# Kernel optimization log

Measured on AMD Instinct MI355X. Metric: run time of the kernel, lower is better.

The kernel has to match this reference:

```python
import jax, jax.numpy as jnp
import numpy as np

B, S, V, E, H, L = 32, 64, 96, 256, 512, 3
DIN = 2 * H  # padded input width for stacked LSTM weight tensors


def _cell(x, h, c, Wih, Whh, bih, bhh):
    # PyTorch LSTMCell gate order: i, f, g, o
    g = x @ Wih.T + h @ Whh.T + bih + bhh
    i, f, gg, o = jnp.split(g, 4, axis=-1)
    c2 = jax.nn.sigmoid(f) * c + jax.nn.sigmoid(i) * jnp.tanh(gg)
    h2 = jax.nn.sigmoid(o) * jnp.tanh(c2)
    return h2, c2


def _pad_feat(x, d):
    p = d - x.shape[-1]
    return x if p == 0 else jnp.pad(x, ((0, 0),) * (x.ndim - 1) + ((0, p),))


def _run_lstm(xs, Wih, Whh, bih, bhh, reverse):
    # xs: [S, B, Din]
    if reverse:
        xs = xs[::-1]
    b = xs.shape[1]
    init = (jnp.zeros((b, H), xs.dtype), jnp.zeros((b, H), xs.dtype))

    def step(carry, xt):
        h, c = _cell(xt, carry[0], carry[1], Wih, Whh, bih, bhh)
        return (h, c), h

    (h, c), ys = jax.lax.scan(step, init, xs)
    if reverse:
        ys = ys[::-1]
    return ys, h, c


def setup_inputs():
    key = jax.random.key(0)
    ks = jax.random.split(key, 20)
    f = lambda k, shp, s=0.08: jax.random.normal(k, shp, jnp.float32) * s
    return {
        "src": jax.random.randint(ks[0], (B, S), 0, V - 1),  # avoids padding_idx=95
        "trg": jax.random.randint(ks[1], (B, S), 0, V - 1),
        "embedding": f(ks[2], (V, E), 0.5),
        "enc_Wih": f(ks[3], (L, 2, 4 * H, DIN)),
        "enc_Whh": f(ks[4], (L, 2, 4 * H, H)),
        "enc_bih": f(ks[5], (L, 2, 4 * H)),
        "enc_bhh": f(ks[6], (L, 2, 4 * H)),
        "dec_Wih": f(ks[7], (L, 4 * H, DIN)),
        "dec_Whh": f(ks[8], (L, 4 * H, H)),
        "dec_bih": f(ks[9], (L, 4 * H)),
        "dec_bhh": f(ks[10], (L, 4 * H)),
        "attn_W": f(ks[11], (H, 3 * H)),
        "attn_b": f(ks[12], (H,)),
        "attn_v": jax.random.uniform(ks[13], (H,), jnp.float32),
        "proj_W": f(ks[14], (2 * H, E + 2 * H)),
        "proj_b": f(ks[15], (2 * H,)),
        "fc_W": f(ks[16], (V, H)),
        "fc_b": f(ks[17], (V,)),
    }


def _forward(src, trg, embedding, enc_Wih, enc_Whh, enc_bih, enc_bhh,
             dec_Wih, dec_Whh, dec_bih, dec_bhh, attn_W, attn_b, attn_v,
             proj_W, proj_b, fc_W, fc_b):
    emb = embedding[src]                 # [B,S,E]; dropout=identity (eval)
    xs = emb.transpose(1, 0, 2)          # [S,B,E]
    h_sum, c_sum = [], []
    for l in range(L):
        xin = _pad_feat(xs, DIN)         # zero-pad so stacked weights apply; padded cols hit zeros
        yf, hf, cf = _run_lstm(xin, enc_Wih[l, 0], enc_Whh[l, 0], enc_bih[l, 0], enc_bhh[l, 0], False)
        yb, hb, cb = _run_lstm(xin, enc_Wih[l, 1], enc_Whh[l, 1], enc_bih[l, 1], enc_bhh[l, 1], True)
        xs = jnp.concatenate([yf, yb], -1)  # [S,B,2H]
        h_sum.append(hf + hb)
        c_sum.append(cf + cb)            # hidden.view(L,2,B,H).sum(dim=1)
    enc_out = xs.transpose(1, 0, 2)      # [B,S,2H]
    dec_h, dec_c = jnp.stack(h_sum), jnp.stack(c_sum)  # [L,B,H]

    tokens = trg[:, :-1].T               # teacher_forcing_ratio = 1.0 (deterministic)

    def dec_step(carry, tok):
        h, c = carry
        htop = h[-1]                     # [B,H]
        rep = jnp.concatenate([jnp.broadcast_to(htop[:, None, :], (B, S, H)), enc_out], -1)
        energy = jnp.tanh(rep @ attn_W.T + attn_b)               # [B,S,H]
        attn = jax.nn.softmax(jnp.einsum('d,bsd->bs', attn_v, energy), axis=1)
        context = jnp.einsum('bs,bsd->bd', attn, enc_out)        # [B,2H]
        x = jnp.concatenate([embedding[tok], context], -1) @ proj_W.T + proj_b  # [B,2H]
        hs, cs = [], []
        xin = x
        for l in range(L):
            hl, cl = _cell(_pad_feat(xin, DIN), h[l], c[l], dec_Wih[l], dec_Whh[l], dec_bih[l], dec_bhh[l])
            hs.append(hl)
            cs.append(cl)
            xin = hl
        out = xin @ fc_W.T + fc_b        # [B,V]
        return (jnp.stack(hs), jnp.stack(cs)), out

    _, outs = jax.lax.scan(dec_step, (dec_h, dec_c), tokens)     # [S-1,B,V]
    outputs = jnp.concatenate([jnp.zeros((1, B, V), outs.dtype), outs], 0)
    return outputs.transpose(1, 0, 2)    # [B,S,V]; t=0 row is zeros, matching torch


def reference(src, trg, embedding, enc_Wih, enc_Whh, enc_bih, enc_bhh,
              dec_Wih, dec_Whh, dec_bih, dec_bhh, attn_W, attn_b, attn_v,
              proj_W, proj_b, fc_W, fc_b):
    return _forward(src, trg, embedding, enc_Wih, enc_Whh, enc_bih, enc_bhh,
                    dec_Wih, dec_Whh, dec_bih, dec_bhh, attn_W, attn_b, attn_v,
                    proj_W, proj_b, fc_W, fc_b)
```

## Files before the change

### kernel.cpp

```cpp
#include <hip/hip_runtime.h>

#define B_ 32
#define S_ 64
#define V_ 96
#define E_ 256
#define H_ 512
#define L_ 3
#define DIN_ 1024
#define G4_ 2048
#define BH_ (B_*H_)
#define BDIN_ (B_*DIN_)
#define FSTRIDE 16

typedef unsigned short u16;
typedef u16 u16x8 __attribute__((ext_vector_type(8)));

__device__ __forceinline__ float bfu(u16 u){ return __uint_as_float(((unsigned)u) << 16); }
__device__ __forceinline__ u16 f2b(float f){
  unsigned x = __float_as_uint(f);
  unsigned r = (x + 0x7FFFu + ((x >> 16) & 1u)) >> 16;
  return (u16)r;
}
__device__ __forceinline__ float sigm(float x){ return 1.f/(1.f+__expf(-x)); }
__device__ __forceinline__ float bsum(float a){
  #pragma unroll
  for(int off=1; off<64; off<<=1) a += __shfl_xor(a, off);
  return a;
}
__device__ __forceinline__ void stc(float* p, float v){
  __hip_atomic_store(p, v, __ATOMIC_RELAXED, __HIP_MEMORY_SCOPE_AGENT);
}
__device__ __forceinline__ float ldc(const float* p){
  return __hip_atomic_load((float*)p, __ATOMIC_RELAXED, __HIP_MEMORY_SCOPE_AGENT);
}
__device__ __forceinline__ void stci(int* p, int v){
  __hip_atomic_store(p, v, __ATOMIC_RELAXED, __HIP_MEMORY_SCOPE_AGENT);
}
__device__ __forceinline__ int ldci(const int* p){
  return __hip_atomic_load((int*)p, __ATOMIC_RELAXED, __HIP_MEMORY_SCOPE_AGENT);
}
template<int BF> __device__ __forceinline__ float LD(const void* p, size_t i){
  if constexpr(BF) return bfu(((const u16*)p)[i]);
  else             return ((const float*)p)[i];
}
template<int BF> __device__ __forceinline__ float4 LD4(const void* p, size_t i){
  if constexpr(BF){
    const u16* q = (const u16*)p + i;
    ushort4 w = *(const ushort4*)q;
    return make_float4(bfu(w.x), bfu(w.y), bfu(w.z), bfu(w.w));
  } else {
    return *(const float4*)((const float*)p + i);
  }
}

__device__ __forceinline__ void gbar(int* flags, int g){
  __syncthreads();
  if(threadIdx.x < 64){
    if(threadIdx.x == 0) stci(&flags[blockIdx.x*FSTRIDE], g);
    const int i0 = threadIdx.x*4;
    for(;;){
      int f0 = ldci(&flags[(i0+0)*FSTRIDE]);
      int f1 = ldci(&flags[(i0+1)*FSTRIDE]);
      int f2 = ldci(&flags[(i0+2)*FSTRIDE]);
      int f3 = ldci(&flags[(i0+3)*FSTRIDE]);
      bool ok = (f0>=g) && (f1>=g) && (f2>=g) && (f3>=g);
      if(__all(ok)) break;
      __builtin_amdgcn_s_sleep(1);
    }
  }
  __syncthreads();
}

__global__ void k_detect(const void* av, int* flag, int* flags){
  __shared__ int cnt;
  if(threadIdx.x == 0) cnt = 0;
  __syncthreads();
  u16 w = ((const u16*)av)[2*threadIdx.x];
  if(w & 0x8000) atomicAdd(&cnt, 1);
  __syncthreads();
  for(int i=threadIdx.x; i<256*FSTRIDE+16; i+=256) flags[i] = 0;
  if(threadIdx.x == 0) *flag = (cnt <= 8) ? 1 : 0;
}

template<int BF> __device__ void embed_body(const int* __restrict__ src,
                                            const void* __restrict__ emb,
                                            float* __restrict__ X0){
  int idx = blockIdx.x*256 + threadIdx.x;
  int d  = idx & (DIN_-1);
  int sb = idx >> 10;
  int b  = sb & (B_-1);
  int s  = sb >> 5;
  float v = 0.f;
  if(d < E_){
    int tok = src[b*S_ + s];
    v = LD<BF>(emb, (size_t)tok*E_ + d);
  }
  X0[idx] = v;
}
__global__ void k_embed(const int* src, const void* emb, float* X0, const int* fl){
  if(*fl) embed_body<1>(src, emb, X0); else embed_body<0>(src, emb, X0);
}

template<int BF> __device__ void gemm_body(
  const float* __restrict__ A, int lda,
  const void* __restrict__ W, int ldw, size_t woff,
  const void* __restrict__ b1, size_t o1,
  const void* __restrict__ b2, size_t o2,
  float* __restrict__ C, int ldc, int K)
{
  __shared__ float As[16][128];
  __shared__ float Bs[16][64];
  const int tid = threadIdx.x;
  const int m0 = blockIdx.y * 128;
  const int n0 = blockIdx.x * 64;
  const int tx = tid & 15, ty = tid >> 4;
  const int amm = tid & 127, akk = (tid >> 7) * 8;
  const int bnn = tid >> 2,  bkk = (tid & 3) * 4;
  float acc[8][4] = {{0.f}};
  for(int k0 = 0; k0 < K; k0 += 16){
    const float4* ap = (const float4*)(A + (size_t)(m0+amm)*lda + (k0 + akk));
    float4 a0 = ap[0];
    float4 a1 = ap[1];
    float4 wv = LD4<BF>(W, woff + (size_t)(n0+bnn)*ldw + (k0 + bkk));
    As[akk+0][amm]=a0.x; As[akk+1][amm]=a0.y; As[akk+2][amm]=a0.z; As[akk+3][amm]=a0.w;
    As[akk+4][amm]=a1.x; As[akk+5][amm]=a1.y; As[akk+6][amm]=a1.z; As[akk+7][amm]=a1.w;
    Bs[bkk+0][bnn]=wv.x; Bs[bkk+1][bnn]=wv.y;
    Bs[bkk+2][bnn]=wv.z; Bs[bkk+3][bnn]=wv.w;
    __syncthreads();
    #pragma unroll
    for(int kk=0;kk<16;kk++){
      const float4 av0 = *(const float4*)&As[kk][ty*8];
      const float4 av1 = *(const float4*)&As[kk][ty*8+4];
      const float4 bv  = *(const float4*)&Bs[kk][tx*4];
      float am[8] = {av0.x,av0.y,av0.z,av0.w,av1.x,av1.y,av1.z,av1.w};
      float bn[4] = {bv.x,bv.y,bv.z,bv.w};
      #pragma unroll
      for(int i=0;i<8;i++){
        #pragma unroll
        for(int j=0;j<4;j++) acc[i][j] = fmaf(am[i], bn[j], acc[i][j]);
      }
    }
    __syncthreads();
  }
  float bias[4];
  #pragma unroll
  for(int j=0;j<4;j++){
    float bb = 0.f;
    if(b1) bb += LD<BF>(b1, o1 + n0 + tx*4 + j);
    if(b2) bb += LD<BF>(b2, o2 + n0 + tx*4 + j);
    bias[j] = bb;
  }
  #pragma unroll
  for(int i=0;i<8;i++){
    float* cp = C + (size_t)(m0 + ty*8 + i)*ldc + (n0 + tx*4);
    #pragma unroll
    for(int j=0;j<4;j++) cp[j] = acc[i][j] + bias[j];
  }
}
__global__ __launch_bounds__(256) void k_gemm(
  const float* A, int lda, const void* W, int ldw, size_t woff,
  const void* b1, size_t o1, const void* b2, size_t o2,
  float* C, int ldc, int K, const int* fl)
{
  if(*fl) gemm_body<1>(A,lda,W,ldw,woff,b1,o1,b2,o2,C,ldc,K);
  else    gemm_body<0>(A,lda,W,ldw,woff,b1,o1,b2,o2,C,ldc,K);
}

__global__ void k_outzero(void* __restrict__ out, const int* fl){
  int i = blockIdx.x*256 + threadIdx.x;
  if(i < B_*V_){
    int b = i / V_, v = i % V_;
    size_t idx = (size_t)b*(S_*V_) + v;
    if(*fl) ((u16*)out)[idx] = 0;
    else    ((float*)out)[idx] = 0.f;
  }
}

struct EncArgs2 {
  const float* G;
  const void* Whh; size_t oWh;
  float* henc;
  float* cT;
  float* Xout;
  float* dh0;
  float* dcT;
  int l;
  const int* fl;
  int* flags; int gbase;
};

template<int BF>
__device__ void enc2_body(const EncArgs2& a){
  __shared__ float SM[16384];
  const int tid  = threadIdx.x;
  const int w    = (blockIdx.x<<2) + (tid>>6);
  const int lane = tid & 63;
  const int d    = w >> 9;
  const int j    = w & 511;
  int g = a.gbase;

  float wh[4][8];
  #pragma unroll
  for(int gg=0; gg<4; gg++){
    size_t rowh = a.oWh + ((size_t)d*G4_ + (size_t)gg*H_ + j)*H_;
    #pragma unroll
    for(int p=0;p<2;p++){
      float4 v = LD4<BF>(a.Whh, rowh + (lane<<2) + p*256);
      wh[gg][p*4+0]=v.x; wh[gg][p*4+1]=v.y; wh[gg][p*4+2]=v.z; wh[gg][p*4+3]=v.w;
    }
  }
  const int bE = lane & 31;
  const size_t ci = ((size_t)d*H_ + j)*32 + bE;
  float cv = 0.f;

  for(int p=0;p<64;p++){
    const int t = d ? (63-p) : p;
    if(p == 0){
      for(int i=tid<<2; i<BH_; i+=1024) *(float4*)&SM[i] = make_float4(0.f,0.f,0.f,0.f);
    } else {
      const float* hsrc = a.henc + (size_t)((p&63)*2 + d)*BH_;
      for(int i=tid<<2; i<BH_; i+=1024) *(float4*)&SM[i] = *(const float4*)&hsrc[i];
    }
    __syncthreads();

    const float* Gp = a.G + (size_t)(t*B_+bE)*4096 + (size_t)d*G4_ + j;
    float pg0=Gp[0], pg1=Gp[512], pg2=Gp[1024], pg3=Gp[1536];

    float gv0=0.f, gv1=0.f, gv2=0.f, gv3=0.f;
    for(int b=0;b<32;b++){
      float gs[4] = {0.f,0.f,0.f,0.f};
      const float* hp = &SM[(b<<9) + (lane<<2)];
      #pragma unroll
      for(int pp=0;pp<2;pp++){
        float4 hv = *(const float4*)(hp + pp*256);
        float ha[4] = {hv.x,hv.y,hv.z,hv.w};
        #pragma unroll
        for(int gg=0;gg<4;gg++){
          #pragma unroll
          for(int i=0;i<4;i++) gs[gg] = fmaf(ha[i], wh[gg][pp*4+i], gs[gg]);
        }
      }
      #pragma unroll
      for(int gg=0;gg<4;gg++) gs[gg] = bsum(gs[gg]);
      if(lane == b){ gv0=gs[0]; gv1=gs[1]; gv2=gs[2]; gv3=gs[3]; }
    }
    if(lane < 32){
      float gi = gv0+pg0, gf = gv1+pg1, gG = gv2+pg2, go = gv3+pg3;
      float c2 = sigm(gf)*cv + sigm(gi)*tanhf(gG);
      float h2 = sigm(go)*tanhf(c2);
      cv = c2;
      stc(&a.henc[(size_t)(((p+1)&63)*2 + d)*BH_ + (size_t)bE*H_ + j], h2);
      a.Xout[(size_t)(t*B_+bE)*DIN_ + (d<<9) + j] = h2;
    }
    gbar(a.flags, ++g);
  }
  if(lane < 32) stc(&a.cT[ci], cv);
  gbar(a.flags, ++g);
  for(int i = blockIdx.x*256 + tid; i < BH_; i += 65536){
    float hf = a.henc[(size_t)(0*2+0)*BH_ + i];
    float hb = a.henc[(size_t)(0*2+1)*BH_ + i];
    a.dh0[(size_t)a.l*BH_ + i] = hf + hb;
    a.dcT[(size_t)a.l*BH_ + i] = ldc(&a.cT[i]) + ldc(&a.cT[BH_ + i]);
  }
}
__global__ __launch_bounds__(256,2) void k_enc2(EncArgs2 a){
  if(*a.fl) enc2_body<1>(a); else enc2_body<0>(a);
}

struct DecArgs2 {
  const int* trg;
  const void* emb; const void* aW; const void* av; const void* pW; const void* pb;
  const void* dWih; const void* dWhh; const void* dbih; const void* dbhh;
  const void* fW; const void* fb;
  const float* Epre; const float* X3;
  const float* dh0;
  float* dhb;
  float* zb;
  u16*   ctxb;
  float* xpb;
  const float* dcT;
  void* out;
  const int* fl;
  int* flags; int gbase;
};

template<int BF, int CP>
__device__ __forceinline__ void dec2_cell(const DecArgs2& a, float* SM,
    const int t, const int l, const int jp, const int bh, const int bh_blk,
    const int lane, const int tid, int& g, float& cv){
  constexpr int Kx = CP*256;
  constexpr int HB = (CP==4) ? 2 : 1;
  constexpr int NB = 16/HB;
  const float* xsrc = (l==0) ? (a.xpb + (size_t)t*BDIN_ + (size_t)bh_blk*16*DIN_)
                             : (a.dhb + (size_t)((t+1)*3 + (l-1))*BH_ + (size_t)bh_blk*16*H_);
  const float* hsrc = (t==0) ? (a.dh0 + (size_t)l*BH_ + (size_t)bh_blk*16*H_)
                             : (a.dhb + (size_t)(t*3 + l)*BH_ + (size_t)bh_blk*16*H_);
  float wx[4][CP*4];
  float wh[4][8];
  #pragma unroll
  for(int gg=0; gg<4; gg++){
    size_t rowx = ((size_t)l*G4_ + (size_t)gg*H_ + jp)*DIN_;
    #pragma unroll
    for(int p=0;p<CP;p++){
      float4 v = LD4<BF>(a.dWih, rowx + (lane<<2) + p*256);
      wx[gg][p*4+0]=v.x; wx[gg][p*4+1]=v.y; wx[gg][p*4+2]=v.z; wx[gg][p*4+3]=v.w;
    }
    size_t rowh = ((size_t)l*G4_ + (size_t)gg*H_ + jp)*H_;
    #pragma unroll
    for(int p=0;p<2;p++){
      float4 v = LD4<BF>(a.dWhh, rowh + (lane<<2) + p*256);
      wh[gg][p*4+0]=v.x; wh[gg][p*4+1]=v.y; wh[gg][p*4+2]=v.z; wh[gg][p*4+3]=v.w;
    }
  }
  float pg[4];
  {
    size_t bb = (size_t)l*G4_ + jp;
    #pragma unroll
    for(int gg=0;gg<4;gg++)
      pg[gg] = LD<BF>(a.dbih, bb + (size_t)gg*H_) + LD<BF>(a.dbhh, bb + (size_t)gg*H_);
  }
  float gv0=0.f,gv1=0.f,gv2=0.f,gv3=0.f;
  #pragma unroll
  for(int hf=0; hf<HB; hf++){
    const float* xg = xsrc + (size_t)hf*NB*Kx;
    const float* hg = hsrc + (size_t)hf*NB*H_;
    for(int i=tid<<2; i<NB*Kx; i+=1024) *(float4*)&SM[i] = *(const float4*)&xg[i];
    for(int i=tid<<2; i<NB*H_; i+=1024) *(float4*)&SM[NB*Kx + i] = *(const float4*)&hg[i];
    __syncthreads();
    for(int ib2=0; ib2<NB; ib2++){
      const int ib = hf*NB + ib2;
      float gs[4] = {0.f,0.f,0.f,0.f};
      const float* xr = &SM[ib2*Kx + (lane<<2)];
      #pragma unroll
      for(int p=0;p<CP;p++){
        float4 xv = *(const float4*)(xr + p*256);
        float xa[4] = {xv.x,xv.y,xv.z,xv.w};
        #pragma unroll
        for(int gg=0;gg<4;gg++){
          #pragma unroll
          for(int i=0;i<4;i++) gs[gg] = fmaf(xa[i], wx[gg][p*4+i], gs[gg]);
        }
      }
      const float* hr = &SM[NB*Kx + ib2*H_ + (lane<<2)];
      #pragma unroll
      for(int p=0;p<2;p++){
        float4 hv = *(const float4*)(hr + p*256);
        float ha[4] = {hv.x,hv.y,hv.z,hv.w};
        #pragma unroll
        for(int gg=0;gg<4;gg++){
          #pragma unroll
          for(int i=0;i<4;i++) gs[gg] = fmaf(ha[i], wh[gg][p*4+i], gs[gg]);
        }
      }
      #pragma unroll
      for(int gg=0;gg<4;gg++) gs[gg] = bsum(gs[gg]);
      if(lane == ib){ gv0=gs[0]; gv1=gs[1]; gv2=gs[2]; gv3=gs[3]; }
    }
    __syncthreads();
  }
  if(lane < 16){
    const int b = bh*16 + lane;
    float gi = gv0+pg[0], gf = gv1+pg[1], gG = gv2+pg[2], go = gv3+pg[3];
    float c2 = sigm(gf)*cv + sigm(gi)*tanhf(gG);
    float h2 = sigm(go)*tanhf(c2);
    cv = c2;
    stc(&a.dhb[(size_t)((t+1)*3 + l)*BH_ + (size_t)b*H_ + jp], h2);
  }
  gbar(a.flags, ++g);
}

template<int BF>
__device__ void dec2_body(const DecArgs2& a){
  __shared__ float SM[16384];
  const int tid  = threadIdx.x;
  const int w    = (blockIdx.x<<2) + (tid>>6);
  const int lane = tid & 63;
  const int jp   = w & 511;
  const int bh   = w >> 9;
  const int bh_blk = blockIdx.x >> 7;
  int g = a.gbase;

  float cvs[3];
  #pragma unroll
  for(int l=0;l<3;l++)
    cvs[l] = a.dcT[((size_t)l*H_ + jp)*32 + (size_t)bh*16 + (lane&15)];

  for(int t=0; t<64; ++t){
    {
      const float* hs = (t==0) ? (a.dh0 + (size_t)2*BH_ + (size_t)bh_blk*16*H_)
                               : (a.dhb + (size_t)(t*3 + 2)*BH_ + (size_t)bh_blk*16*H_);
      for(int i=tid<<2; i<16*H_; i+=1024) *(float4*)&SM[i] = *(const float4*)&hs[i];
      __syncthreads();
      if(t < 63){
        float wz[8];
        size_t rz = (size_t)jp*1536;
        #pragma unroll
        for(int p=0;p<2;p++){
          float4 v = LD4<BF>(a.aW, rz + (lane<<2) + p*256);
          wz[p*4+0]=v.x; wz[p*4+1]=v.y; wz[p*4+2]=v.z; wz[p*4+3]=v.w;
        }
        for(int ib=0; ib<16; ib++){
          const float* hp = &SM[(ib<<9) + (lane<<2)];
          float acc = 0.f;
          #pragma unroll
          for(int p=0;p<2;p++){
            float4 hv = *(const float4*)(hp + p*256);
            acc = fmaf(hv.x, wz[p*4+0], acc); acc = fmaf(hv.y, wz[p*4+1], acc);
            acc = fmaf(hv.z, wz[p*4+2], acc); acc = fmaf(hv.w, wz[p*4+3], acc);
          }
          acc = bsum(acc);
          if(lane==0) stc(&a.zb[(size_t)t*BH_ + (size_t)(bh*16+ib)*H_ + jp], acc);
        }
      }
      if(t > 0){
        #pragma unroll
        for(int r=0;r<3;r++){
          const int q  = jp + (r<<9);
          const int v_ = q % 96;
          const int ib = q / 96;
          float wf[8];
          size_t rf = (size_t)v_*H_;
          #pragma unroll
          for(int p=0;p<2;p++){
            float4 v = LD4<BF>(a.fW, rf + (lane<<2) + p*256);
            wf[p*4+0]=v.x; wf[p*4+1]=v.y; wf[p*4+2]=v.z; wf[p*4+3]=v.w;
          }
          const float* hp = &SM[(ib<<9) + (lane<<2)];
          float acc = 0.f;
          #pragma unroll
          for(int p=0;p<2;p++){
            float4 hv = *(const float4*)(hp + p*256);
            acc = fmaf(hv.x, wf[p*4+0], acc); acc = fmaf(hv.y, wf[p*4+1], acc);
            acc = fmaf(hv.z, wf[p*4+2], acc); acc = fmaf(hv.w, wf[p*4+3], acc);
          }
          acc = bsum(acc);
          if(lane==0){
            float rr = acc + LD<BF>(a.fb, v_);
            size_t oi = (size_t)(bh*16+ib)*(S_*V_) + (size_t)t*V_ + v_;
            if constexpr(BF) ((u16*)a.out)[oi] = f2b(rr);
            else             ((float*)a.out)[oi] = rr;
          }
        }
      }
    }
    if(t == 63) break;
    gbar(a.flags, ++g);

    if(blockIdx.x < 32){
      const int b = blockIdx.x;
      float* Zs = SM; float* Ss = SM + 512;
      for(int i=tid; i<512; i+=256) Zs[i] = a.zb[(size_t)t*BH_ + (size_t)b*H_ + i];
      __syncthreads();
      float wa[8];
      #pragma unroll
      for(int p=0;p<2;p++){
        float4 v = LD4<BF>(a.av, (lane<<2) + p*256);
        wa[p*4+0]=v.x; wa[p*4+1]=v.y; wa[p*4+2]=v.z; wa[p*4+3]=v.w;
      }
      const int ww = tid>>6;
      for(int s=ww; s<64; s+=4){
        const float* ep = a.Epre + ((size_t)(s*B_ + b))*H_;
        float acc = 0.f;
        #pragma unroll
        for(int p=0;p<2;p++){
          const float4 e4 = *(const float4*)(ep + (lane<<2) + p*256);
          const float4 z4 = *(const float4*)(Zs + (lane<<2) + p*256);
          acc = fmaf(wa[p*4+0], tanhf(e4.x+z4.x), acc);
          acc = fmaf(wa[p*4+1], tanhf(e4.y+z4.y), acc);
          acc = fmaf(wa[p*4+2], tanhf(e4.z+z4.z), acc);
          acc = fmaf(wa[p*4+3], tanhf(e4.w+z4.w), acc);
        }
        acc = bsum(acc);
        if(lane==0) Ss[s] = acc;
      }
      __syncthreads();
      if(tid < 64){
        float vv = Ss[tid];
        float m = vv;
        #pragma unroll
        for(int off=1; off<64; off<<=1) m = fmaxf(m, __shfl_xor(m, off));
        float e = __expf(vv - m);
        float su = e;
        #pragma unroll
        for(int off=1; off<64; off<<=1) su += __shfl_xor(su, off);
        Ss[tid] = e / su;
      }
      __syncthreads();
      for(int d4 = tid<<2; d4 < DIN_; d4 += 1024){
        float a0=0.f,a1=0.f,a2=0.f,a3=0.f;
        const float* xb = a.X3 + (size_t)b*DIN_ + d4;
        for(int s=0;s<64;s++){
          const float pp = Ss[s];
          const float4 xv = *(const float4*)(xb + (size_t)s*BDIN_);
          a0 = fmaf(pp, xv.x, a0); a1 = fmaf(pp, xv.y, a1);
          a2 = fmaf(pp, xv.z, a2); a3 = fmaf(pp, xv.w, a3);
        }
        u16* cp = a.ctxb + (size_t)t*BDIN_ + (size_t)b*DIN_ + d4;
        unsigned lo = (unsigned)f2b(a0) | ((unsigned)f2b(a1)<<16);
        unsigned hi = (unsigned)f2b(a2) | ((unsigned)f2b(a3)<<16);
        stci((int*)cp, (int)lo);
        stci(((int*)cp)+1, (int)hi);
      }
    }
    gbar(a.flags, ++g);

    {
      const u16* cs = a.ctxb + (size_t)t*BDIN_ + (size_t)bh_blk*16*DIN_;
      for(int i=tid*8; i<16*DIN_; i+=2048){
        u16x8 v = *(const u16x8*)(cs + i);
        #pragma unroll
        for(int k=0;k<8;k++) SM[i+k] = bfu(v[k]);
      }
      __syncthreads();
      float wpe[2][4], wpc[2][16];
      #pragma unroll
      for(int jj=0;jj<2;jj++){
        size_t row = (size_t)(jp + (jj<<9))*1280;
        float4 v = LD4<BF>(a.pW, row + (lane<<2));
        wpe[jj][0]=v.x; wpe[jj][1]=v.y; wpe[jj][2]=v.z; wpe[jj][3]=v.w;
        #pragma unroll
        for(int p=0;p<4;p++){
          float4 c4 = LD4<BF>(a.pW, row + 256 + (lane<<2) + p*256);
          wpc[jj][p*4+0]=c4.x; wpc[jj][p*4+1]=c4.y; wpc[jj][p*4+2]=c4.z; wpc[jj][p*4+3]=c4.w;
        }
      }
      const float pb0 = LD<BF>(a.pb, jp);
      const float pb1 = LD<BF>(a.pb, jp+512);
      for(int ib=0; ib<16; ib++){
        const int b = bh*16 + ib;
        const int tok = a.trg[b*S_ + t];
        float4 ev = LD4<BF>(a.emb, (size_t)tok*E_ + (lane<<2));
        float ea[4] = {ev.x, ev.y, ev.z, ev.w};
        float s0=0.f, s1=0.f;
        #pragma unroll
        for(int i=0;i<4;i++){ s0 = fmaf(ea[i], wpe[0][i], s0); s1 = fmaf(ea[i], wpe[1][i], s1); }
        const float* cp = &SM[(ib<<10) + (lane<<2)];
        #pragma unroll
        for(int p=0;p<4;p++){
          float4 c4 = *(const float4*)(cp + p*256);
          float ca[4] = {c4.x,c4.y,c4.z,c4.w};
          #pragma unroll
          for(int i=0;i<4;i++){ s0 = fmaf(ca[i], wpc[0][p*4+i], s0); s1 = fmaf(ca[i], wpc[1][p*4+i], s1); }
        }
        s0 = bsum(s0); s1 = bsum(s1);
        if(lane==0){
          stc(&a.xpb[(size_t)t*BDIN_ + (size_t)b*DIN_ + jp],       s0 + pb0);
          stc(&a.xpb[(size_t)t*BDIN_ + (size_t)b*DIN_ + jp + 512], s1 + pb1);
        }
      }
    }
    gbar(a.flags, ++g);

    dec2_cell<BF,4>(a, SM, t, 0, jp, bh, bh_blk, lane, tid, g, cvs[0]);
    dec2_cell<BF,2>(a, SM, t, 1, jp, bh, bh_blk, lane, tid, g, cvs[1]);
    dec2_cell<BF,2>(a, SM, t, 2, jp, bh, bh_blk, lane, tid, g, cvs[2]);
  }
}
__global__ __launch_bounds__(256,2) void k_dec2(DecArgs2 a){
  if(*a.fl) dec2_body<1>(a); else dec2_body<0>(a);
}

struct EncArgsO {
  const float* G;
  const float* Xin;
  const void* Wih; size_t oWi;
  const void* Whh; size_t oWh;
  const void* bih; size_t obi;
  const void* bhh; size_t obh;
  float* hst; float* cT; float* Xout; float* dh; float* dcT;
  int l; const int* fl; int* flags; int gbase;
};

template<int BF, int CP>
__device__ void encO_body(const EncArgsO& a){
  __shared__ float SM[16384];
  const int tid  = threadIdx.x;
  const int w    = (blockIdx.x<<2) + (tid>>6);
  const int lane = tid & 63;
  const int d    = w >> 9;
  const int j    = w & 511;
  int g = a.gbase;

  float wh[4][8];
  #pragma unroll
  for(int gg=0; gg<4; gg++){
    size_t rowh = a.oWh + ((size_t)d*G4_ + (size_t)gg*H_ + j)*H_;
    #pragma unroll
    for(int p=0;p<2;p++){
      float4 v = LD4<BF>(a.Whh, rowh + (lane<<2) + p*256);
      wh[gg][p*4+0]=v.x; wh[gg][p*4+1]=v.y; wh[gg][p*4+2]=v.z; wh[gg][p*4+3]=v.w;
    }
  }
  float wxf[4][CP?CP*4:1];
  float pbias[4];
  if constexpr(CP>0){
    #pragma unroll
    for(int gg=0; gg<4; gg++){
      size_t rowx = a.oWi + ((size_t)d*G4_ + (size_t)gg*H_ + j)*DIN_;
      #pragma unroll
      for(int p=0;p<CP;p++){
        float4 v = LD4<BF>(a.Wih, rowx + (lane<<2) + p*256);
        wxf[gg][p*4+0]=v.x; wxf[gg][p*4+1]=v.y; wxf[gg][p*4+2]=v.z; wxf[gg][p*4+3]=v.w;
      }
    }
    size_t bb = (size_t)d*G4_ + j;
    #pragma unroll
    for(int gg=0;gg<4;gg++)
      pbias[gg] = LD<BF>(a.bih, a.obi + bb + (size_t)gg*H_)
                + LD<BF>(a.bhh, a.obh + bb + (size_t)gg*H_);
  }
  const int bE = lane & 31;
  const size_t ci = ((size_t)d*H_ + j)*32 + bE;
  float cv = 0.f;
  int cur = 0;
  for(int p=0;p<64;p++){
    const int t = d ? (63-p) : p;
    if(p == 0){
      for(int i=tid<<2; i<BH_; i+=1024) *(float4*)&SM[i] = make_float4(0.f,0.f,0.f,0.f);
    } else {
      const float* hsrc = a.hst + (size_t)((cur<<1)+d)*BH_;
      #pragma unroll 4
      for(int i=tid; i<BH_; i+=256) SM[i] = ldc(hsrc + i);
    }
    __syncthreads();
    float pg[4];
    if constexpr(CP==0){
      const float* Gp = a.G + (size_t)(t*B_+bE)*4096 + (size_t)d*G4_ + j;
      pg[0]=Gp[0]; pg[1]=Gp[512]; pg[2]=Gp[1024]; pg[3]=Gp[1536];
    } else {
      pg[0]=pbias[0]; pg[1]=pbias[1]; pg[2]=pbias[2]; pg[3]=pbias[3];
    }
    const float* xrow = nullptr;
    if constexpr(CP>0) xrow = a.Xin + (size_t)t*B_*DIN_;
    float gv0=0.f, gv1=0.f, gv2=0.f, gv3=0.f;
    for(int b=0;b<32;b++){
      float gs[4] = {0.f,0.f,0.f,0.f};
      const float* hp = &SM[(b<<9) + (lane<<2)];
      #pragma unroll
      for(int pp=0;pp<2;pp++){
        float4 hv = *(const float4*)(hp + pp*256);
        float ha[4] = {hv.x,hv.y,hv.z,hv.w};
        #pragma unroll
        for(int gg=0;gg<4;gg++){
          #pragma unroll
          for(int i=0;i<4;i++) gs[gg] = fmaf(ha[i], wh[gg][pp*4+i], gs[gg]);
        }
      }
      if constexpr(CP>0){
        const float* xr = xrow + (size_t)b*DIN_ + (lane<<2);
        #pragma unroll
        for(int pp=0;pp<CP;pp++){
          float4 xv = *(const float4*)(xr + pp*256);
          float xa[4] = {xv.x,xv.y,xv.z,xv.w};
          #pragma unroll
          for(int gg=0;gg<4;gg++){
            #pragma unroll
            for(int i=0;i<4;i++) gs[gg] = fmaf(xa[i], wxf[gg][pp*4+i], gs[gg]);
          }
        }
      }
      #pragma unroll
      for(int gg=0;gg<4;gg++) gs[gg] = bsum(gs[gg]);
      if(lane == b){ gv0=gs[0]; gv1=gs[1]; gv2=gs[2]; gv3=gs[3]; }
    }
    if(lane < 32){
      float gi = gv0+pg[0], gf = gv1+pg[1], gG = gv2+pg[2], go = gv3+pg[3];
      float c2 = sigm(gf)*cv + sigm(gi)*tanhf(gG);
      float h2 = sigm(go)*tanhf(c2);
      cv = c2;
      stc(&a.hst[(size_t)(((cur^1)<<1)+d)*BH_ + (size_t)bE*H_ + j], h2);
      a.Xout[(size_t)(t*B_+bE)*DIN_ + (d<<9) + j] = h2;
    }
    gbar(a.flags, ++g);
    cur ^= 1;
  }
  if(lane < 32) stc(&a.cT[ci], cv);
  gbar(a.flags, ++g);
  for(int i = blockIdx.x*256 + tid; i < BH_; i += 65536){
    a.dh[(size_t)a.l*BH_ + i]  = ldc(&a.hst[(size_t)(cur<<1)*BH_ + i])
                               + ldc(&a.hst[(size_t)((cur<<1)+1)*BH_ + i]);
    a.dcT[(size_t)a.l*BH_ + i] = ldc(&a.cT[i]) + ldc(&a.cT[BH_ + i]);
  }
}
__global__ __launch_bounds__(256,2) void k_enc_persF0(EncArgsO a){
  if(*a.fl) encO_body<1,1>(a); else encO_body<0,1>(a);
}
__global__ __launch_bounds__(256,2) void k_enc_persF12(EncArgsO a){
  if(*a.fl) encO_body<1,4>(a); else encO_body<0,4>(a);
}

struct DecArgsO {
  const int* trg;
  const void* emb; const void* aW; const void* av; const void* pW; const void* pb;
  const void* dWih; const void* dWhh; const void* dbih; const void* dbhh;
  const void* fW; const void* fb;
  const float* Epre; const float* X3;
  float* dh; float* dcT; float* z; float* ctx; float* xp;
  void* out; const int* fl; int* flags; int gbase;
};

template<int BF, int CP>
__device__ __forceinline__ void decO_cell(const DecArgsO& a, float* SM,
    const int l, const int cur, const int jp, const int bh, const int bh_blk,
    const int lane, const int tid, int& g, float& cv){
  constexpr int Kx = CP*256;
  constexpr int HB = (CP==4) ? 2 : 1;
  constexpr int NB = 16/HB;
  const float* xsrc = (l==0) ? (a.xp + (size_t)bh_blk*16*DIN_)
                             : (a.dh + ((size_t)(cur^1)*3 + (l-1))*BH_ + (size_t)bh_blk*16*H_);
  const float* hsrc = a.dh + ((size_t)cur*3 + l)*BH_ + (size_t)bh_blk*16*H_;
  float wx[4][CP*4];
// ... 166 lines not shown
        for(int p=0;p<2;p++){
          const float4 e4 = *(const float4*)(ep + (lane<<2) + p*256);
          const float4 z4 = *(const float4*)(Zs + (lane<<2) + p*256);
          acc = fmaf(wa[p*4+0], tanhf(e4.x+z4.x), acc);
          acc = fmaf(wa[p*4+1], tanhf(e4.y+z4.y), acc);
          acc = fmaf(wa[p*4+2], tanhf(e4.z+z4.z), acc);
          acc = fmaf(wa[p*4+3], tanhf(e4.w+z4.w), acc);
        }
        acc = bsum(acc);
        if(lane==0) Ss[s] = acc;
      }
      __syncthreads();
      if(tid < 64){
        float vv = Ss[tid];
        float m = vv;
        #pragma unroll
        for(int off=1; off<64; off<<=1) m = fmaxf(m, __shfl_xor(m, off));
        float e = __expf(vv - m);
        float su = e;
        #pragma unroll
        for(int off=1; off<64; off<<=1) su += __shfl_xor(su, off);
        Ss[tid] = e / su;
      }
      __syncthreads();
      for(int d4 = tid<<2; d4 < DIN_; d4 += 1024){
        float a0=0.f,a1=0.f,a2=0.f,a3=0.f;
        const float* xb = a.X3 + (size_t)b*DIN_ + d4;
        for(int s=0;s<64;s++){
          const float pp = Ss[s];
          const float4 xv = *(const float4*)(xb + (size_t)s*BDIN_);
          a0 = fmaf(pp, xv.x, a0); a1 = fmaf(pp, xv.y, a1);
          a2 = fmaf(pp, xv.z, a2); a3 = fmaf(pp, xv.w, a3);
        }
        float* cp = &a.ctx[(size_t)b*DIN_ + d4];
        stc(cp+0, a0); stc(cp+1, a1); stc(cp+2, a2); stc(cp+3, a3);
      }
    }
    gbar(a.flags, ++g);
    {
      const float* cs = a.ctx + (size_t)bh_blk*16*DIN_;
      #pragma unroll 4
      for(int i=tid; i<16*DIN_; i+=256) SM[i] = ldc(cs + i);
      __syncthreads();
      float wpe[2][4], wpc[2][16];
      #pragma unroll
      for(int jj=0;jj<2;jj++){
        size_t row = (size_t)(jp + (jj<<9))*1280;
        float4 v = LD4<BF>(a.pW, row + (lane<<2));
        wpe[jj][0]=v.x; wpe[jj][1]=v.y; wpe[jj][2]=v.z; wpe[jj][3]=v.w;
        #pragma unroll
        for(int p=0;p<4;p++){
          float4 c4 = LD4<BF>(a.pW, row + 256 + (lane<<2) + p*256);
          wpc[jj][p*4+0]=c4.x; wpc[jj][p*4+1]=c4.y; wpc[jj][p*4+2]=c4.z; wpc[jj][p*4+3]=c4.w;
        }
      }
      const float pb0 = LD<BF>(a.pb, jp);
      const float pb1 = LD<BF>(a.pb, jp+512);
      for(int ib=0; ib<16; ib++){
        const int b = bh*16 + ib;
        const int tok = a.trg[b*S_ + t];
        float4 ev = LD4<BF>(a.emb, (size_t)tok*E_ + (lane<<2));
        float ea[4] = {ev.x, ev.y, ev.z, ev.w};
        float s0=0.f, s1=0.f;
        #pragma unroll
        for(int i=0;i<4;i++){ s0 = fmaf(ea[i], wpe[0][i], s0); s1 = fmaf(ea[i], wpe[1][i], s1); }
        const float* cp = &SM[(ib<<10) + (lane<<2)];
        #pragma unroll
        for(int p=0;p<4;p++){
          float4 c4 = *(const float4*)(cp + p*256);
          float ca[4] = {c4.x,c4.y,c4.z,c4.w};
          #pragma unroll
          for(int i=0;i<4;i++){ s0 = fmaf(ca[i], wpc[0][p*4+i], s0); s1 = fmaf(ca[i], wpc[1][p*4+i], s1); }
        }
        s0 = bsum(s0); s1 = bsum(s1);
        if(lane==0){
          stc(&a.xp[(size_t)b*DIN_ + jp],       s0 + pb0);
          stc(&a.xp[(size_t)b*DIN_ + jp + 512], s1 + pb1);
        }
      }
    }
    gbar(a.flags, ++g);
    decO_cell<BF,4>(a, SM, 0, cur, jp, bh, bh_blk, lane, tid, g, cvs[0]);
    decO_cell<BF,2>(a, SM, 1, cur, jp, bh, bh_blk, lane, tid, g, cvs[1]);
    decO_cell<BF,2>(a, SM, 2, cur, jp, bh, bh_blk, lane, tid, g, cvs[2]);
    cur ^= 1;
  }
}
__global__ __launch_bounds__(256,2) void k_dec_persO(DecArgsO a){
  if(*a.fl) decO_body<1>(a); else decO_body<0>(a);
}

extern "C" void kernel_launch(void* const* d_in, const int* in_sizes, int n_in,
                              void* d_out, int out_size, void* d_ws, size_t ws_size,
                              hipStream_t stream){
  const int* src  = (const int*)d_in[0];
  const int* trg  = (const int*)d_in[1];
  const void* emb = d_in[2];
  const void* eWih= d_in[3];
  const void* eWhh= d_in[4];
  const void* ebih= d_in[5];
  const void* ebhh= d_in[6];
  const void* dWih= d_in[7];
  const void* dWhh= d_in[8];
  const void* dbih= d_in[9];
  const void* dbhh= d_in[10];
  const void* aW  = d_in[11];
  const void* ab  = d_in[12];
  const void* av  = d_in[13];
  const void* pW  = d_in[14];
  const void* pb  = d_in[15];
  const void* fW  = d_in[16];
  const void* fb  = d_in[17];

  char* base = (char*)d_ws;
  size_t off = 0;
  auto take = [&](size_t bytes)->char*{
    char* p = base + off; off = (off + bytes + 255) & ~(size_t)255; return p;
  };

  const size_t szX  = (size_t)2048*1024*4;
  const size_t szG  = (size_t)2048*4096*4;
  const size_t szE  = (size_t)2048*512*4;
  int planA = ws_size >= (size_t)53*1024*1024;

  if(planA){
    float* X    = (float*)take(szX);
    float* Xh   = (float*)take(szX);
    float* G    = (float*)take(szG);
    float* dhb  = G;
    float* zb   = dhb + (size_t)64*3*BH_;
    float* xpb  = zb  + (size_t)63*BH_;
    u16*   ctxb = (u16*)(xpb + (size_t)63*BDIN_);
    float* Epre = (float*)take(szE);
    float* cTe  = (float*)take((size_t)2*BH_*4);
    float* dh0  = (float*)take((size_t)3*BH_*4);
    float* dcT  = (float*)take((size_t)3*BH_*4);
    int* fl     = (int*)take(256);
    int* flags  = (int*)take((256*FSTRIDE + 16)*4);

    k_detect<<<1, 256, 0, stream>>>(av, fl, flags);
    k_embed<<<8192, 256, 0, stream>>>(src, emb, X, fl);

    for(int l=0;l<L_;l++){
      int K = (l==0) ? E_ : DIN_;
      k_gemm<<<dim3(64,16), 256, 0, stream>>>(X, DIN_,
          eWih, DIN_, (size_t)l*2*G4_*DIN_,
          ebih, (size_t)l*2*G4_, ebhh, (size_t)l*2*G4_,
          G, 4096, K, fl);
      EncArgs2 ea;
      ea.G = G; ea.Whh = eWhh; ea.oWh = (size_t)l*2*G4_*H_;
      ea.henc = Xh; ea.cT = cTe; ea.Xout = X;
      ea.dh0 = dh0; ea.dcT = dcT; ea.l = l;
      ea.fl = fl; ea.flags = flags; ea.gbase = l*65;
      k_enc2<<<256, 256, 0, stream>>>(ea);
    }
    k_gemm<<<dim3(8,16), 256, 0, stream>>>(X, DIN_,
        aW, 3*H_, (size_t)H_, ab, 0, nullptr, 0, Epre, H_, DIN_, fl);
    k_outzero<<<12, 256, 0, stream>>>(d_out, fl);

    DecArgs2 da;
    da.trg = trg; da.emb = emb; da.aW = aW; da.av = av; da.pW = pW; da.pb = pb;
    da.dWih = dWih; da.dWhh = dWhh; da.dbih = dbih; da.dbhh = dbhh;
    da.fW = fW; da.fb = fb;
    da.Epre = Epre; da.X3 = X;
    da.dh0 = dh0; da.dhb = dhb; da.zb = zb; da.ctxb = ctxb; da.xpb = xpb;
    da.dcT = dcT; da.out = d_out; da.fl = fl; da.flags = flags; da.gbase = 3*65;
    k_dec2<<<256, 256, 0, stream>>>(da);
  } else {
    float* XA   = (float*)take(szX);
    float* XB   = (float*)take(szX);
    float* Epre = (float*)take(szE);
    float* hst  = (float*)take((size_t)4*BH_*4);
    float* cTe  = (float*)take((size_t)2*BH_*4);
    float* dh   = (float*)take((size_t)6*BH_*4);
    float* dcT  = (float*)take((size_t)3*BH_*4);
    float* zbuf = (float*)take((size_t)BH_*4);
    float* ctx  = (float*)take((size_t)2*BH_*4);
    float* xp   = (float*)take((size_t)2*BH_*4);
    int* fl     = (int*)take(256);
    int* flags  = (int*)take((256*FSTRIDE + 16)*4);

    k_detect<<<1, 256, 0, stream>>>(av, fl, flags);
    k_embed<<<8192, 256, 0, stream>>>(src, emb, XA, fl);

    float* Xin = XA; float* Xout = XB;
    for(int l=0;l<L_;l++){
      int K = (l==0) ? E_ : DIN_;
      EncArgsO ea;
      ea.G = nullptr; ea.Xin = Xin;
      ea.Wih = eWih; ea.oWi = (size_t)l*2*G4_*DIN_;
      ea.Whh = eWhh; ea.oWh = (size_t)l*2*G4_*H_;
      ea.bih = ebih; ea.obi = (size_t)l*2*G4_;
      ea.bhh = ebhh; ea.obh = (size_t)l*2*G4_;
      ea.hst = hst; ea.cT = cTe; ea.Xout = Xout;
      ea.dh = dh; ea.dcT = dcT; ea.l = l;
      ea.fl = fl; ea.flags = flags; ea.gbase = l*65;
      if(l == 0) k_enc_persF0<<<256, 256, 0, stream>>>(ea);
      else       k_enc_persF12<<<256, 256, 0, stream>>>(ea);
      float* tmp = Xin; Xin = Xout; Xout = tmp;
      (void)K;
    }
    k_gemm<<<dim3(8,16), 256, 0, stream>>>(Xin, DIN_,
        aW, 3*H_, (size_t)H_, ab, 0, nullptr, 0, Epre, H_, DIN_, fl);
    k_outzero<<<12, 256, 0, stream>>>(d_out, fl);

    DecArgsO da;
    da.trg = trg; da.emb = emb; da.aW = aW; da.av = av; da.pW = pW; da.pb = pb;
    da.dWih = dWih; da.dWhh = dWhh; da.dbih = dbih; da.dbhh = dbhh;
    da.fW = fW; da.fb = fb;
    da.Epre = Epre; da.X3 = Xin;
    da.dh = dh; da.dcT = dcT; da.z = zbuf; da.ctx = ctx; da.xp = xp;
    da.out = d_out; da.fl = fl; da.flags = flags; da.gbase = 3*65;
    k_dec_persO<<<256, 256, 0, stream>>>(da);
  }
}
```

Before: 11.46 ms.

## Double block size in persistent encoder/decoder, splitting batch rows across wave halves

```diff
diff --git a/kernel.cpp b/kernel.cpp
--- a/kernel.cpp
+++ b/kernel.cpp
@@ -13,7 +13,6 @@
 #define FSTRIDE 16
 
 typedef unsigned short u16;
-typedef u16 u16x8 __attribute__((ext_vector_type(8)));
 
 __device__ __forceinline__ float bfu(u16 u){ return __uint_as_float(((unsigned)u) << 16); }
 __device__ __forceinline__ u16 f2b(float f){
@@ -193,10 +192,12 @@
 __device__ void enc2_body(const EncArgs2& a){
   __shared__ float SM[16384];
   const int tid  = threadIdx.x;
-  const int w    = (blockIdx.x<<2) + (tid>>6);
   const int lane = tid & 63;
-  const int d    = w >> 9;
-  const int j    = w & 511;
+  const int wid  = tid >> 6;
+  const int w4   = (blockIdx.x<<2) + (wid & 3);
+  const int j    = w4 & 511;
+  const int d    = w4 >> 9;
+  const int half = wid >> 2;
   int g = a.gbase;
 
   float wh[4][8];
@@ -209,25 +210,26 @@
       wh[gg][p*4+0]=v.x; wh[gg][p*4+1]=v.y; wh[gg][p*4+2]=v.z; wh[gg][p*4+3]=v.w;
     }
   }
-  const int bE = lane & 31;
-  const size_t ci = ((size_t)d*H_ + j)*32 + bE;
+  const bool own = (lane < 32) && ((lane>>4) == half);
+  const size_t ci = ((size_t)d*H_ + j)*32 + (lane & 31);
   float cv = 0.f;
 
   for(int p=0;p<64;p++){
     const int t = d ? (63-p) : p;
     if(p == 0){
-      for(int i=tid<<2; i<BH_; i+=1024) *(float4*)&SM[i] = make_float4(0.f,0.f,0.f,0.f);
+      for(int i=tid<<2; i<BH_; i+=2048) *(float4*)&SM[i] = make_float4(0.f,0.f,0.f,0.f);
     } else {
       const float* hsrc = a.henc + (size_t)((p&63)*2 + d)*BH_;
-      for(int i=tid<<2; i<BH_; i+=1024) *(float4*)&SM[i] = *(const float4*)&hsrc[i];
+      for(int i=tid<<2; i<BH_; i+=2048) *(float4*)&SM[i] = *(const float4*)&hsrc[i];
     }
     __syncthreads();
 
+    const int bE = lane & 31;
     const float* Gp = a.G + (size_t)(t*B_+bE)*4096 + (size_t)d*G4_ + j;
     float pg0=Gp[0], pg1=Gp[512], pg2=Gp[1024], pg3=Gp[1536];
 
     float gv0=0.f, gv1=0.f, gv2=0.f, gv3=0.f;
-    for(int b=0;b<32;b++){
+    for(int b=half*16; b<half*16+16; b++){
       float gs[4] = {0.f,0.f,0.f,0.f};
       const float* hp = &SM[(b<<9) + (lane<<2)];
       #pragma unroll
@@ -244,26 +246,26 @@
       for(int gg=0;gg<4;gg++) gs[gg] = bsum(gs[gg]);
       if(lane == b){ gv0=gs[0]; gv1=gs[1]; gv2=gs[2]; gv3=gs[3]; }
     }
-    if(lane < 32){
+    if(own){
       float gi = gv0+pg0, gf = gv1+pg1, gG = gv2+pg2, go = gv3+pg3;
       float c2 = sigm(gf)*cv + sigm(gi)*tanhf(gG);
       float h2 = sigm(go)*tanhf(c2);
       cv = c2;
-      stc(&a.henc[(size_t)(((p+1)&63)*2 + d)*BH_ + (size_t)bE*H_ + j], h2);
-      a.Xout[(size_t)(t*B_+bE)*DIN_ + (d<<9) + j] = h2;
+      stc(&a.henc[(size_t)(((p+1)&63)*2 + d)*BH_ + (size_t)lane*H_ + j], h2);
+      a.Xout[(size_t)(t*B_+lane)*DIN_ + (d<<9) + j] = h2;
     }
     gbar(a.flags, ++g);
   }
-  if(lane < 32) stc(&a.cT[ci], cv);
+  if(own) stc(&a.cT[ci], cv);
   gbar(a.flags, ++g);
-  for(int i = blockIdx.x*256 + tid; i < BH_; i += 65536){
-    float hf = a.henc[(size_t)(0*2+0)*BH_ + i];
-    float hb = a.henc[(size_t)(0*2+1)*BH_ + i];
-    a.dh0[(size_t)a.l*BH_ + i] = hf + hb;
+  for(int i = blockIdx.x*512 + tid; i < BH_; i += 131072){
+    float hf2 = a.henc[(size_t)(0*2+0)*BH_ + i];
+    float hb2 = a.henc[(size_t)(0*2+1)*BH_ + i];
+    a.dh0[(size_t)a.l*BH_ + i] = hf2 + hb2;
     a.dcT[(size_t)a.l*BH_ + i] = ldc(&a.cT[i]) + ldc(&a.cT[BH_ + i]);
   }
 }
-__global__ __launch_bounds__(256,2) void k_enc2(EncArgs2 a){
+__global__ __launch_bounds__(512,1) void k_enc2(EncArgs2 a){
   if(*a.fl) enc2_body<1>(a); else enc2_body<0>(a);
 }
 
@@ -287,10 +289,11 @@
 template<int BF, int CP>
 __device__ __forceinline__ void dec2_cell(const DecArgs2& a, float* SM,
     const int t, const int l, const int jp, const int bh, const int bh_blk,
-    const int lane, const int tid, int& g, float& cv){
-  constexpr int Kx = CP*256;
-  constexpr int HB = (CP==4) ? 2 : 1;
-  constexpr int NB = 16/HB;
+    const int lane, const int tid, const int half, int& g, float& cv){
+  constexpr int Kx  = CP*256;
+  constexpr int HB  = (CP==4) ? 2 : 1;
+  constexpr int NBs = 16/HB;
+  constexpr int NW  = NBs/2;
   const float* xsrc = (l==0) ? (a.xpb + (size_t)t*BDIN_ + (size_t)bh_blk*16*DIN_)
                              : (a.dhb + (size_t)((t+1)*3 + (l-1))*BH_ + (size_t)bh_blk*16*H_);
   const float* hsrc = (t==0) ? (a.dh0 + (size_t)l*BH_ + (size_t)bh_blk*16*H_)
@@ -322,13 +325,13 @@
   float gv0=0.f,gv1=0.f,gv2=0.f,gv3=0.f;
   #pragma unroll
   for(int hf=0; hf<HB; hf++){
-    const float* xg = xsrc + (size_t)hf*NB*Kx;
-    const float* hg = hsrc + (size_t)hf*NB*H_;
-    for(int i=tid<<2; i<NB*Kx; i+=1024) *(float4*)&SM[i] = *(const float4*)&xg[i];
-    for(int i=tid<<2; i<NB*H_; i+=1024) *(float4*)&SM[NB*Kx + i] = *(const float4*)&hg[i];
+    const float* xg = xsrc + (size_t)hf*NBs*Kx;
+    const float* hg = hsrc + (size_t)hf*NBs*H_;
+    for(int i=tid<<2; i<NBs*Kx; i+=2048) *(float4*)&SM[i] = *(const float4*)&xg[i];
+    for(int i=tid<<2; i<NBs*H_; i+=2048) *(float4*)&SM[NBs*Kx + i] = *(const float4*)&hg[i];
     __syncthreads();
-    for(int ib2=0; ib2<NB; ib2++){
-      const int ib = hf*NB + ib2;
+    for(int ib2=half*NW; ib2<half*NW+NW; ib2++){
+      const int ib = hf*NBs + ib2;
       float gs[4] = {0.f,0.f,0.f,0.f};
       const float* xr = &SM[ib2*Kx + (lane<<2)];
       #pragma unroll
@@ -341,7 +344,7 @@
           for(int i=0;i<4;i++) gs[gg] = fmaf(xa[i], wx[gg][p*4+i], gs[gg]);
         }
       }
-      const float* hr = &SM[NB*Kx + ib2*H_ + (lane<<2)];
+      const float* hr = &SM[NBs*Kx + ib2*H_ + (lane<<2)];
       #pragma unroll
       for(int p=0;p<2;p++){
         float4 hv = *(const float4*)(hr + p*256);
@@ -358,7 +361,8 @@
     }
     __syncthreads();
   }
-  if(lane < 16){
+  const bool own = (lane < 16) && (((CP==4) ? ((lane>>2)&1) : (lane>>3)) == half);
+  if(own){
     const int b = bh*16 + lane;
     float gi = gv0+pg[0], gf = gv1+pg[1], gG = gv2+pg[2], go = gv3+pg[3];
     float c2 = sigm(gf)*cv + sigm(gi)*tanhf(gG);
@@ -373,10 +377,12 @@
 __device__ void dec2_body(const DecArgs2& a){
   __shared__ float SM[16384];
   const int tid  = threadIdx.x;
-  const int w    = (blockIdx.x<<2) + (tid>>6);
   const int lane = tid & 63;
-  const int jp   = w & 511;
-  const int bh   = w >> 9;
+  const int wid  = tid >> 6;
+  const int w4   = (blockIdx.x<<2) + (wid & 3);
+  const int jp   = w4 & 511;
+  const int bh   = w4 >> 9;
+  const int half = wid >> 2;
   const int bh_blk = blockIdx.x >> 7;
   int g = a.gbase;
 
@@ -389,7 +395,7 @@
     {
       const float* hs = (t==0) ? (a.dh0 + (size_t)2*BH_ + (size_t)bh_blk*16*H_)
                                : (a.dhb + (size_t)(t*3 + 2)*BH_ + (size_t)bh_blk*16*H_);
-      for(int i=tid<<2; i<16*H_; i+=1024) *(float4*)&SM[i] = *(const float4*)&hs[i];
+      for(int i=tid<<2; i<16*H_; i+=2048) *(float4*)&SM[i] = *(const float4*)&hs[i];
       __syncthreads();
       if(t < 63){
         float wz[8];
@@ -399,7 +405,7 @@
           float4 v = LD4<BF>(a.aW, rz + (lane<<2) + p*256);
           wz[p*4+0]=v.x; wz[p*4+1]=v.y; wz[p*4+2]=v.z; wz[p*4+3]=v.w;
         }
-        for(int ib=0; ib<16; ib++){
+        for(int ib=half*8; ib<half*8+8; ib++){
           const float* hp = &SM[(ib<<9) + (lane<<2)];
           float acc = 0.f;
           #pragma unroll
@@ -418,6 +424,7 @@
           const int q  = jp + (r<<9);
           const int v_ = q % 96;
           const int ib = q / 96;
+          if((ib>>3) != half) continue;
           float wf[8];
           size_t rf = (size_t)v_*H_;
           #pragma unroll
@@ -449,7 +456,7 @@
     if(blockIdx.x < 32){
       const int b = blockIdx.x;
       float* Zs = SM; float* Ss = SM + 512;
-      for(int i=tid; i<512; i+=256) Zs[i] = a.zb[(size_t)t*BH_ + (size_t)b*H_ + i];
+      for(int i=tid; i<512; i+=512) Zs[i] = a.zb[(size_t)t*BH_ + (size_t)b*H_ + i];
       __syncthreads();
       float wa[8];
       #pragma unroll
@@ -457,8 +464,7 @@
         float4 v = LD4<BF>(a.av, (lane<<2) + p*256);
         wa[p*4+0]=v.x; wa[p*4+1]=v.y; wa[p*4+2]=v.z; wa[p*4+3]=v.w;
       }
-      const int ww = tid>>6;
-      for(int s=ww; s<64; s+=4){
+      for(int s=wid; s<64; s+=8){
         const float* ep = a.Epre + ((size_t)(s*B_ + b))*H_;
         float acc = 0.f;
         #pragma unroll
@@ -486,7 +492,7 @@
         Ss[tid] = e / su;
       }
       __syncthreads();
-      for(int d4 = tid<<2; d4 < DIN_; d4 += 1024){
+      for(int d4 = tid<<2; d4 < DIN_; d4 += 2048){
         float a0=0.f,a1=0.f,a2=0.f,a3=0.f;
         const float* xb = a.X3 + (size_t)b*DIN_ + d4;
         for(int s=0;s<64;s++){
@@ -506,10 +512,9 @@
 
     {
       const u16* cs = a.ctxb + (size_t)t*BDIN_ + (size_t)bh_blk*16*DIN_;
-      for(int i=tid*8; i<16*DIN_; i+=2048){
-        u16x8 v = *(const u16x8*)(cs + i);
-        #pragma unroll
-        for(int k=0;k<8;k++) SM[i+k] = bfu(v[k]);
+      for(int i=tid*4; i<16*DIN_; i+=2048){
+        ushort4 v = *(const ushort4*)(cs + i);
+        *(float4*)&SM[i] = make_float4(bfu(v.x), bfu(v.y), bfu(v.z), bfu(v.w));
       }
       __syncthreads();
       float wpe[2][4], wpc[2][16];
@@ -526,7 +531,7 @@
       }
       const float pb0 = LD<BF>(a.pb, jp);
       const float pb1 = LD<BF>(a.pb, jp+512);
-      for(int ib=0; ib<16; ib++){
+      for(int ib=half*8; ib<half*8+8; ib++){
         const int b = bh*16 + ib;
         const int tok = a.trg[b*S_ + t];
         float4 ev = LD4<BF>(a.emb, (size_t)tok*E_ + (lane<<2));
@@ -548,15 +553,16 @@
           stc(&a.xpb[(size_t)t*BDIN_ + (size_t)b*DIN_ + jp + 512], s1 + pb1);
         }
       }
+      __syncthreads();
     }
     gbar(a.flags, ++g);
 
-    dec2_cell<BF,4>(a, SM, t, 0, jp, bh, bh_blk, lane, tid, g, cvs[0]);
-    dec2_cell<BF,2>(a, SM, t, 1, jp, bh, bh_blk, lane, tid, g, cvs[1]);
-    dec2_cell<BF,2>(a, SM, t, 2, jp, bh, bh_blk, lane, tid, g, cvs[2]);
-  }
-}
-__global__ __launch_bounds__(256,2) void k_dec2(DecArgs2 a){
+    dec2_cell<BF,4>(a, SM, t, 0, jp, bh, bh_blk, lane, tid, half, g, cvs[0]);
+    dec2_cell<BF,2>(a, SM, t, 1, jp, bh, bh_blk, lane, tid, half, g, cvs[1]);
+    dec2_cell<BF,2>(a, SM, t, 2, jp, bh, bh_blk, lane, tid, half, g, cvs[2]);
+  }
+}
+__global__ __launch_bounds__(512,1) void k_dec2(DecArgs2 a){
   if(*a.fl) dec2_body<1>(a); else dec2_body<0>(a);
 }
 
@@ -1029,7 +1035,7 @@
       ea.henc = Xh; ea.cT = cTe; ea.Xout = X;
       ea.dh0 = dh0; ea.dcT = dcT; ea.l = l;
       ea.fl = fl; ea.flags = flags; ea.gbase = l*65;
-      k_enc2<<<256, 256, 0, stream>>>(ea);
+      k_enc2<<<256, 512, 0, stream>>>(ea);
     }
     k_gemm<<<dim3(8,16), 256, 0, stream>>>(X, DIN_,
         aW, 3*H_, (size_t)H_, ab, 0, nullptr, 0, Epre, H_, DIN_, fl);
@@ -1042,7 +1048,7 @@
     da.Epre = Epre; da.X3 = X;
     da.dh0 = dh0; da.dhb = dhb; da.zb = zb; da.ctxb = ctxb; da.xpb = xpb;
     da.dcT = dcT; da.out = d_out; da.fl = fl; da.flags = flags; da.gbase = 3*65;
-    k_dec2<<<256, 256, 0, stream>>>(da);
+    k_dec2<<<256, 512, 0, stream>>>(da);
   } else {
     float* XA   = (float*)take(szX);
     float* XB   = (float*)take(szX);
@@ -1062,7 +1068,6 @@
 
     float* Xin = XA; float* Xout = XB;
     for(int l=0;l<L_;l++){
-      int K = (l==0) ? E_ : DIN_;
       EncArgsO ea;
       ea.G = nullptr; ea.Xin = Xin;
       ea.Wih = eWih; ea.oWi = (size_t)l*2*G4_*DIN_;
@@ -1075,7 +1080,6 @@
       if(l == 0) k_enc_persF0<<<256, 256, 0, stream>>>(ea);
       else       k_enc_persF12<<<256, 256, 0, stream>>>(ea);
       float* tmp = Xin; Xin = Xout; Xout = tmp;
-      (void)K;
     }
     k_gemm<<<dim3(8,16), 256, 0, stream>>>(Xin, DIN_,
         aW, 3*H_, (size_t)H_, ab, 0, nullptr, 0, Epre, H_, DIN_, fl);
```

After: 10.47 ms. 1.09x faster.
